# Optimization experiments

Measured on AMD Instinct MI355X. Metric: run time of the kernel, lower is better.

## Reference

```python
import jax, jax.numpy as jnp
import numpy as np


def setup_inputs() -> dict:
    key = jax.random.key(0)
    k1, k2, k3, k4 = jax.random.split(key, 4)
    B, T, L, C, F = 1024, 128, 256, 2, 784
    x = jax.random.normal(k1, (B, T, F), dtype=jnp.float32)
    W = jax.random.normal(k2, (L, F), dtype=jnp.float32) * (1.0 / np.sqrt(F))
    b = jax.random.normal(k3, (L,), dtype=jnp.float32) * 0.01
    contribution = jax.random.normal(k4, (T, L, C), dtype=jnp.float32)
    return {"x": x, "W": W, "b": b, "contribution": contribution}


def reference(x, W, b, contribution):
    # symbolic_paths: Linear(784 -> leaf) + Hardtanh  -> [B, T, L]
    sp = jnp.clip(jnp.einsum('btf,lf->btl', x, W) + b, -1.0, 1.0)
    # per-(tree,leaf) outer product: class_value[b,t,l,c] = sp[b,t,l] * contribution[t,l,c]
    cv = sp[..., None] * contribution[None]          # [B, T, L, C]
    p = jax.nn.softmax(cv, axis=-1)                  # softmax over classes
    gini = jnp.sum(1.0 - p * p, axis=-1)             # [B, T, L]
    return (sp, gini)
```

## Files before the change

### kernel.cpp

```cpp
#include <hip/hip_runtime.h>
#include <hip/hip_bf16.h>

typedef __attribute__((ext_vector_type(8))) short bf16x8;
typedef __attribute__((ext_vector_type(4))) float f32x4;

#define B_SZ   1024
#define T_SZ   128
#define L_SZ   256
#define F_SZ   784
#define M_TOT  (B_SZ * T_SZ)
#define BK     32
#define KSTEPS 25
#define KCHUNKS 100
#define BROWS  32

#define WPRE_ELEMS (KSTEPS * 4 * L_SZ)
#define WPRE_BYTES (WPRE_ELEMS * 16)
#define CDIFF_ELEMS (T_SZ * L_SZ)
#define WS_NEED (WPRE_BYTES + CDIFF_ELEMS * 4)

__device__ __forceinline__ unsigned short f2bf(float f) {
    __hip_bfloat16 h = __float2bfloat16(f);
    return *reinterpret_cast<unsigned short*>(&h);
}

__global__ __launch_bounds__(256) void dn_prep(
    const float* __restrict__ W, const float* __restrict__ contrib,
    unsigned short* __restrict__ wpre, float* __restrict__ cdiff)
{
    const int gid = blockIdx.x * 256 + threadIdx.x;
    if (gid < WPRE_ELEMS) {
        const int leaf = gid & 255;
        const int kg   = (gid >> 8) & 3;
        const int ks   = gid >> 10;
        const int k0   = ks * BK + kg * 8;
        bf16x8 v;
        #pragma unroll
        for (int j = 0; j < 8; ++j) {
            const int k = k0 + j;
            const float f = (k < F_SZ) ? W[(size_t)leaf * F_SZ + k] : 0.f;
            v[j] = (short)f2bf(f);
        }
        *reinterpret_cast<bf16x8*>(wpre + (size_t)gid * 8) = v;
    } else {
        const int cid = gid - WPRE_ELEMS;
        if (cid < CDIFF_ELEMS)
            cdiff[cid] = contrib[(size_t)cid * 2] - contrib[(size_t)cid * 2 + 1];
    }
}

__global__ __launch_bounds__(512, 6) void dn_fused7(
    const float* __restrict__ x, const unsigned short* __restrict__ wpre,
    const float* __restrict__ bias, const float* __restrict__ cdiff,
    float* __restrict__ out)
{
    __shared__ __align__(16) unsigned char smem[KCHUNKS * BROWS * 16];
    bf16x8* As = reinterpret_cast<bf16x8*>(smem);
    typedef float OtRow[264];
    OtRow* Ot = reinterpret_cast<OtRow*>(smem);

    const int tid  = threadIdx.x;
    const int lane = tid & 63;
    const int wid  = tid >> 6;
    const int lr   = lane & 15;
    const int kseg = lane >> 4;

    const int rowBase = blockIdx.x * BROWS;
    const int colBase = wid * 32;

    #pragma unroll
    for (int it = 0; it < 7; ++it) {
        const int i = it * 512 + tid;
        if (i < BROWS * KCHUNKS) {
            const int row = i / KCHUNKS;
            const int kc  = i - row * KCHUNKS;
            bf16x8 v;
            if (kc < 98) {
                const float* p = x + (size_t)(rowBase + row) * F_SZ + kc * 8;
                const f32x4 lo = *reinterpret_cast<const f32x4*>(p);
                const f32x4 hi = *reinterpret_cast<const f32x4*>(p + 4);
                #pragma unroll
                for (int j = 0; j < 4; ++j) {
                    v[j]     = (short)f2bf(lo[j]);
                    v[4 + j] = (short)f2bf(hi[j]);
                }
            } else {
                #pragma unroll
                for (int j = 0; j < 8; ++j) v[j] = 0;
            }
            As[kc * BROWS + (row ^ (kc & 7))] = v;
        }
    }
    __syncthreads();

    const unsigned short* wpb = wpre + ((size_t)kseg * L_SZ + colBase + lr) * 8;

    f32x4 acc[2][2];
    #pragma unroll
    for (int mi = 0; mi < 2; ++mi)
        #pragma unroll
        for (int ni = 0; ni < 2; ++ni)
            acc[mi][ni] = (f32x4){0.f, 0.f, 0.f, 0.f};

    bf16x8 wcur[2], wnxt[2];
    wcur[0] = *reinterpret_cast<const bf16x8*>(wpb);
    wcur[1] = *reinterpret_cast<const bf16x8*>(wpb + 128);

    #pragma unroll
    for (int ks = 0; ks < KSTEPS; ++ks) {
        if (ks + 1 < KSTEPS) {
            wnxt[0] = *reinterpret_cast<const bf16x8*>(wpb + (size_t)(ks + 1) * 8192);
            wnxt[1] = *reinterpret_cast<const bf16x8*>(wpb + (size_t)(ks + 1) * 8192 + 128);
        }
        const int kcr = ks * 4 + kseg;
        const bf16x8 a0 = As[kcr * BROWS + (lr ^ (kcr & 7))];
        const bf16x8 a1 = As[kcr * BROWS + ((16 + lr) ^ (kcr & 7))];

        acc[0][0] = __builtin_amdgcn_mfma_f32_16x16x32_bf16(a0, wcur[0], acc[0][0], 0, 0, 0);
        acc[0][1] = __builtin_amdgcn_mfma_f32_16x16x32_bf16(a0, wcur[1], acc[0][1], 0, 0, 0);
        acc[1][0] = __builtin_amdgcn_mfma_f32_16x16x32_bf16(a1, wcur[0], acc[1][0], 0, 0, 0);
        acc[1][1] = __builtin_amdgcn_mfma_f32_16x16x32_bf16(a1, wcur[1], acc[1][1], 0, 0, 0);

        wcur[0] = wnxt[0];
        wcur[1] = wnxt[1];
    }
    __syncthreads();

    float spv[2][2][4];
    #pragma unroll
    for (int ni = 0; ni < 2; ++ni) {
        const float bb = bias[colBase + ni * 16 + lr];
        #pragma unroll
        for (int mi = 0; mi < 2; ++mi)
            #pragma unroll
            for (int r = 0; r < 4; ++r)
                spv[mi][ni][r] = fminf(fmaxf(acc[mi][ni][r] + bb, -1.f), 1.f);
    }

    const int erow = tid >> 4;
    const int ecol = (tid & 15) * 4;
    const size_t GOFF = (size_t)M_TOT * L_SZ;
    float* orow = out + (size_t)(rowBase + erow) * L_SZ;

    #pragma unroll
    for (int ni = 0; ni < 2; ++ni)
        #pragma unroll
        for (int mi = 0; mi < 2; ++mi)
            #pragma unroll
            for (int r = 0; r < 4; ++r)
                Ot[mi * 16 + kseg * 4 + r][colBase + ni * 16 + lr] = spv[mi][ni][r];
    __syncthreads();
    #pragma unroll
    for (int j = 0; j < 4; ++j) {
        const f32x4 v = *reinterpret_cast<const f32x4*>(&Ot[erow][ecol + 64 * j]);
        *reinterpret_cast<f32x4*>(orow + ecol + 64 * j) = v;
    }
    __syncthreads();

    #pragma unroll
    for (int ni = 0; ni < 2; ++ni) {
        const int col = colBase + ni * 16 + lr;
        #pragma unroll
        for (int mi = 0; mi < 2; ++mi)
            #pragma unroll
            for (int r = 0; r < 4; ++r) {
                const int t = (rowBase + mi * 16 + kseg * 4 + r) & (T_SZ - 1);
                const float d  = spv[mi][ni][r] * cdiff[t * L_SZ + col];
                const float ed = __expf(d);
                const float s2 = ed / (1.f + ed);
                Ot[mi * 16 + kseg * 4 + r][col] = fmaf(2.f * s2, 1.f - s2, 1.f);
            }
    }
    __syncthreads();
    #pragma unroll
    for (int j = 0; j < 4; ++j) {
        const f32x4 v = *reinterpret_cast<const f32x4*>(&Ot[erow][ecol + 64 * j]);
        *reinterpret_cast<f32x4*>(orow + GOFF + ecol + 64 * j) = v;
    }
}

__global__ __launch_bounds__(512) void dn_fused_v1(
    const float* __restrict__ x, const float* __restrict__ W,
    const float* __restrict__ bias, const float* __restrict__ contrib,
    float* __restrict__ out)
{
    __shared__ bf16x8 As[4][128];
    __shared__ bf16x8 Bs[4][L_SZ];

    const int tid    = threadIdx.x;
    const int lane   = tid & 63;
    const int wid    = tid >> 6;
    const int waveM  = wid >> 2;
    const int waveN  = wid & 3;
    const int blkRow = blockIdx.x * 128;
    const int ar = tid >> 2;
    const int ak = (tid & 3) * 8;
    const int wr = tid >> 1;
    const int wk = (tid & 1) * 16;
    const int laneRow = lane & 15;
    const int kgrp    = lane >> 4;

    f32x4 acc[4][4];
    #pragma unroll
    for (int i = 0; i < 4; ++i)
        #pragma unroll
        for (int j = 0; j < 4; ++j)
            acc[i][j] = (f32x4){0.f, 0.f, 0.f, 0.f};

    const float* xrow = x + (size_t)(blkRow + ar) * F_SZ;
    const float* wrow = W + (size_t)wr * F_SZ;
    const f32x4 zf = {0.f, 0.f, 0.f, 0.f};

    f32x4 xa0 = *reinterpret_cast<const f32x4*>(xrow + ak);
    f32x4 xa1 = *reinterpret_cast<const f32x4*>(xrow + ak + 4);
    f32x4 wa0 = *reinterpret_cast<const f32x4*>(wrow + wk);
    f32x4 wa1 = *reinterpret_cast<const f32x4*>(wrow + wk + 4);
    f32x4 wa2 = *reinterpret_cast<const f32x4*>(wrow + wk + 8);
    f32x4 wa3 = *reinterpret_cast<const f32x4*>(wrow + wk + 12);

    for (int ks = 0; ks < KSTEPS; ++ks) {
        bf16x8 av, wv0, wv1;
        #pragma unroll
        for (int j = 0; j < 4; ++j) {
            av[j]      = (short)f2bf(xa0[j]);
            av[4 + j]  = (short)f2bf(xa1[j]);
            wv0[j]     = (short)f2bf(wa0[j]);
            wv0[4 + j] = (short)f2bf(wa1[j]);
            wv1[j]     = (short)f2bf(wa2[j]);
            wv1[4 + j] = (short)f2bf(wa3[j]);
        }
        As[ak >> 3][ar] = av;
        Bs[wk >> 3][wr] = wv0;
        Bs[(wk >> 3) + 1][wr] = wv1;
        __syncthreads();

        if (ks + 1 < KSTEPS) {
            const int kb = (ks + 1) * BK;
            if (kb + ak < F_SZ) {
                xa0 = *reinterpret_cast<const f32x4*>(xrow + kb + ak);
                xa1 = *reinterpret_cast<const f32x4*>(xrow + kb + ak + 4);
            } else { xa0 = zf; xa1 = zf; }
            if (kb + wk < F_SZ) {
                wa0 = *reinterpret_cast<const f32x4*>(wrow + kb + wk);
                wa1 = *reinterpret_cast<const f32x4*>(wrow + kb + wk + 4);
                wa2 = *reinterpret_cast<const f32x4*>(wrow + kb + wk + 8);
                wa3 = *reinterpret_cast<const f32x4*>(wrow + kb + wk + 12);
            } else { wa0 = zf; wa1 = zf; wa2 = zf; wa3 = zf; }
        }

        bf16x8 af[4], bfv[4];
        #pragma unroll
        for (int mi = 0; mi < 4; ++mi)
            af[mi] = As[kgrp][waveM * 64 + mi * 16 + laneRow];
        #pragma unroll
        for (int ni = 0; ni < 4; ++ni)
            bfv[ni] = Bs[kgrp][waveN * 64 + ni * 16 + laneRow];
        #pragma unroll
        for (int mi = 0; mi < 4; ++mi)
            #pragma unroll
            for (int ni = 0; ni < 4; ++ni)
                acc[mi][ni] = __builtin_amdgcn_mfma_f32_16x16x32_bf16(
                    af[mi], bfv[ni], acc[mi][ni], 0, 0, 0);
        __syncthreads();
    }

    const size_t GOFF  = (size_t)M_TOT * L_SZ;
    const int    rbase = waveM * 64 + (lane >> 4) * 4;
    const int    cbase = waveN * 64 + laneRow;
    #pragma unroll
    for (int ni = 0; ni < 4; ++ni) {
        const int col = cbase + ni * 16;
        const float bb = bias[col];
        #pragma unroll
        for (int mi = 0; mi < 4; ++mi) {
            #pragma unroll
            for (int r = 0; r < 4; ++r) {
                const int m = blkRow + rbase + mi * 16 + r;
                const int t = m & (T_SZ - 1);
                float v  = acc[mi][ni][r] + bb;
                float sp = fminf(fmaxf(v, -1.f), 1.f);
                const float* cp = contrib + (size_t)(t * L_SZ + col) * 2;
                const float d  = sp * (cp[0] - cp[1]);
                const float ed = __expf(d);
                const float s  = ed / (1.f + ed);
                const float g  = fmaf(2.f * s, 1.f - s, 1.f);
                const size_t o = (size_t)m * L_SZ + col;
                out[o]        = sp;
                out[GOFF + o] = g;
            }
        }
    }
}

extern "C" void kernel_launch(void* const* d_in, const int* in_sizes, int n_in,
                              void* d_out, int out_size, void* d_ws, size_t ws_size,
                              hipStream_t stream) {
    const float* x       = (const float*)d_in[0];
    const float* W       = (const float*)d_in[1];
    const float* bias    = (const float*)d_in[2];
    const float* contrib = (const float*)d_in[3];
    float* out = (float*)d_out;

    if (ws_size >= (size_t)WS_NEED && d_ws != nullptr) {
        unsigned short* wpre  = (unsigned short*)d_ws;
        float*          cdiff = (float*)((char*)d_ws + WPRE_BYTES);
        const int prep_threads = WPRE_ELEMS + CDIFF_ELEMS;
        dn_prep<<<(prep_threads + 255) / 256, 256, 0, stream>>>(W, contrib, wpre, cdiff);
        dn_fused7<<<M_TOT / BROWS, 512, 0, stream>>>(x, wpre, bias, cdiff, out);
    } else {
        dn_fused_v1<<<M_TOT / 128, 512, 0, stream>>>(x, W, bias, contrib, out);
    }
}
```

Baseline: 186.5 us.

## Warp-specialize fused kernel: producer waves stage x tiles, consumer waves run MFMA

Replaces the 512-thread single-tile kernel with a 1024-thread block that handles 128 rows in four 32-row stages. Eight producer waves convert x to bf16 into a double-buffered LDS tile while eight consumer waves run the MFMA GEMM and epilogue on the previous buffer. Each consumer wave writes its output through a small private slab, so no block-wide sync is needed for the transpose. The goal is to overlap global x loads and conversion with compute. In exchange it uses about 117 KB of LDS, which limits occupancy to one block per CU, and half the waves never issue MFMA.

```diff
diff --git a/kernel.cpp b/kernel.cpp
--- a/kernel.cpp
+++ b/kernel.cpp
@@ -12,12 +12,16 @@
 #define BK     32
 #define KSTEPS 25
 #define KCHUNKS 100
-#define BROWS  32
 
 #define WPRE_ELEMS (KSTEPS * 4 * L_SZ)
 #define WPRE_BYTES (WPRE_ELEMS * 16)
 #define CDIFF_ELEMS (T_SZ * L_SZ)
 #define WS_NEED (WPRE_BYTES + CDIFF_ELEMS * 4)
+
+#define BUFB     51200
+#define SLAB_OFF 102400
+#define SLABB    2176
+#define SMEM_SZ  119808
 
 __device__ __forceinline__ unsigned short f2bf(float f) {
     __hip_bfloat16 h = __float2bfloat16(f);
@@ -49,34 +53,28 @@
     }
 }
 
-__global__ __launch_bounds__(512, 6) void dn_fused7(
+__global__ __launch_bounds__(1024, 4) void dn_fused15(
     const float* __restrict__ x, const unsigned short* __restrict__ wpre,
     const float* __restrict__ bias, const float* __restrict__ cdiff,
     float* __restrict__ out)
 {
-    __shared__ __align__(16) unsigned char smem[KCHUNKS * BROWS * 16];
-    bf16x8* As = reinterpret_cast<bf16x8*>(smem);
-    typedef float OtRow[264];
-    OtRow* Ot = reinterpret_cast<OtRow*>(smem);
-
-    const int tid  = threadIdx.x;
-    const int lane = tid & 63;
-    const int wid  = tid >> 6;
-    const int lr   = lane & 15;
-    const int kseg = lane >> 4;
-
-    const int rowBase = blockIdx.x * BROWS;
-    const int colBase = wid * 32;
-
-    #pragma unroll
-    for (int it = 0; it < 7; ++it) {
-        const int i = it * 512 + tid;
-        if (i < BROWS * KCHUNKS) {
+    __shared__ __align__(16) unsigned char smem[SMEM_SZ];
+
+    const int tid    = threadIdx.x;
+    const int lane   = tid & 63;
+    const int wid    = tid >> 6;
+    const int rowBlk = blockIdx.x * 128;
+    const size_t GOFF = (size_t)M_TOT * L_SZ;
+
+    auto STAGE = [&](int st) {
+        bf16x8* As = reinterpret_cast<bf16x8*>(smem + (size_t)(st & 1) * BUFB);
+        const size_t rb = (size_t)(rowBlk + st * 32);
+        for (int i = wid * 64 + lane; i < 32 * KCHUNKS; i += 512) {
             const int row = i / KCHUNKS;
             const int kc  = i - row * KCHUNKS;
             bf16x8 v;
             if (kc < 98) {
-                const float* p = x + (size_t)(rowBase + row) * F_SZ + kc * 8;
+                const float* p = x + (rb + row) * F_SZ + kc * 8;
                 const f32x4 lo = *reinterpret_cast<const f32x4*>(p);
                 const f32x4 hi = *reinterpret_cast<const f32x4*>(p + 4);
                 #pragma unroll
@@ -88,94 +86,110 @@
                 #pragma unroll
                 for (int j = 0; j < 8; ++j) v[j] = 0;
             }
-            As[kc * BROWS + (row ^ (kc & 7))] = v;
-        }
-    }
+            As[kc * 32 + (row ^ (kc & 7))] = v;
+        }
+    };
+
+    const int cw      = wid - 8;
+    const int colBase = cw * 32;
+    const int lr      = lane & 15;
+    const int kseg    = lane >> 4;
+    const unsigned short* wpb =
+        wpre + ((size_t)kseg * L_SZ + colBase + lr) * 8;
+    float* slab = reinterpret_cast<float*>(smem + SLAB_OFF + cw * SLABB);
+    const int erow8 = lane >> 3;
+    const int ecol  = (lane & 7) * 4;
+
+    if (wid < 8) STAGE(0);
     __syncthreads();
 
-    const unsigned short* wpb = wpre + ((size_t)kseg * L_SZ + colBase + lr) * 8;
-
-    f32x4 acc[2][2];
-    #pragma unroll
-    for (int mi = 0; mi < 2; ++mi)
-        #pragma unroll
-        for (int ni = 0; ni < 2; ++ni)
-            acc[mi][ni] = (f32x4){0.f, 0.f, 0.f, 0.f};
-
-    bf16x8 wcur[2], wnxt[2];
-    wcur[0] = *reinterpret_cast<const bf16x8*>(wpb);
-    wcur[1] = *reinterpret_cast<const bf16x8*>(wpb + 128);
-
-    #pragma unroll
-    for (int ks = 0; ks < KSTEPS; ++ks) {
-        if (ks + 1 < KSTEPS) {
-            wnxt[0] = *reinterpret_cast<const bf16x8*>(wpb + (size_t)(ks + 1) * 8192);
-            wnxt[1] = *reinterpret_cast<const bf16x8*>(wpb + (size_t)(ks + 1) * 8192 + 128);
-        }
-        const int kcr = ks * 4 + kseg;
-        const bf16x8 a0 = As[kcr * BROWS + (lr ^ (kcr & 7))];
-        const bf16x8 a1 = As[kcr * BROWS + ((16 + lr) ^ (kcr & 7))];
-
-        acc[0][0] = __builtin_amdgcn_mfma_f32_16x16x32_bf16(a0, wcur[0], acc[0][0], 0, 0, 0);
-        acc[0][1] = __builtin_amdgcn_mfma_f32_16x16x32_bf16(a0, wcur[1], acc[0][1], 0, 0, 0);
-        acc[1][0] = __builtin_amdgcn_mfma_f32_16x16x32_bf16(a1, wcur[0], acc[1][0], 0, 0, 0);
-        acc[1][1] = __builtin_amdgcn_mfma_f32_16x16x32_bf16(a1, wcur[1], acc[1][1], 0, 0, 0);
-
-        wcur[0] = wnxt[0];
-        wcur[1] = wnxt[1];
-    }
-    __syncthreads();
-
-    float spv[2][2][4];
-    #pragma unroll
-    for (int ni = 0; ni < 2; ++ni) {
-        const float bb = bias[colBase + ni * 16 + lr];
-        #pragma unroll
-        for (int mi = 0; mi < 2; ++mi)
-            #pragma unroll
-            for (int r = 0; r < 4; ++r)
-                spv[mi][ni][r] = fminf(fmaxf(acc[mi][ni][r] + bb, -1.f), 1.f);
-    }
-
-    const int erow = tid >> 4;
-    const int ecol = (tid & 15) * 4;
-    const size_t GOFF = (size_t)M_TOT * L_SZ;
-    float* orow = out + (size_t)(rowBase + erow) * L_SZ;
-
-    #pragma unroll
-    for (int ni = 0; ni < 2; ++ni)
-        #pragma unroll
-        for (int mi = 0; mi < 2; ++mi)
-            #pragma unroll
-            for (int r = 0; r < 4; ++r)
-                Ot[mi * 16 + kseg * 4 + r][colBase + ni * 16 + lr] = spv[mi][ni][r];
-    __syncthreads();
-    #pragma unroll
-    for (int j = 0; j < 4; ++j) {
-        const f32x4 v = *reinterpret_cast<const f32x4*>(&Ot[erow][ecol + 64 * j]);
-        *reinterpret_cast<f32x4*>(orow + ecol + 64 * j) = v;
-    }
-    __syncthreads();
-
-    #pragma unroll
-    for (int ni = 0; ni < 2; ++ni) {
-        const int col = colBase + ni * 16 + lr;
-        #pragma unroll
-        for (int mi = 0; mi < 2; ++mi)
-            #pragma unroll
-            for (int r = 0; r < 4; ++r) {
-                const int t = (rowBase + mi * 16 + kseg * 4 + r) & (T_SZ - 1);
-                const float d  = spv[mi][ni][r] * cdiff[t * L_SZ + col];
-                const float ed = __expf(d);
-                const float s2 = ed / (1.f + ed);
-                Ot[mi * 16 + kseg * 4 + r][col] = fmaf(2.f * s2, 1.f - s2, 1.f);
-            }
-    }
-    __syncthreads();
-    #pragma unroll
-    for (int j = 0; j < 4; ++j) {
-        const f32x4 v = *reinterpret_cast<const f32x4*>(&Ot[erow][ecol + 64 * j]);
-        *reinterpret_cast<f32x4*>(orow + GOFF + ecol + 64 * j) = v;
+    for (int st = 0; st < 4; ++st) {
+        if (wid < 8) {
+            if (st < 3) STAGE(st + 1);
+        } else {
+            const unsigned char* Ab = smem + (size_t)(st & 1) * BUFB;
+            f32x4 acc[2][2];
+            #pragma unroll
+            for (int mi = 0; mi < 2; ++mi)
+                #pragma unroll
+                for (int ni = 0; ni < 2; ++ni)
+                    acc[mi][ni] = (f32x4){0.f, 0.f, 0.f, 0.f};
+
+            bf16x8 wcur[2], wnxt[2];
+            wcur[0] = *reinterpret_cast<const bf16x8*>(wpb);
+            wcur[1] = *reinterpret_cast<const bf16x8*>(wpb + 128);
+
+            #pragma unroll
+            for (int ks = 0; ks < KSTEPS; ++ks) {
+                if (ks + 1 < KSTEPS) {
+                    wnxt[0] = *reinterpret_cast<const bf16x8*>(wpb + (size_t)(ks + 1) * 8192);
+                    wnxt[1] = *reinterpret_cast<const bf16x8*>(wpb + (size_t)(ks + 1) * 8192 + 128);
+                }
+                const int kcr = ks * 4 + kseg;
+                const bf16x8 a0 = *reinterpret_cast<const bf16x8*>(
+                    Ab + (size_t)(kcr * 32 + (lr ^ (kcr & 7))) * 16);
+                const bf16x8 a1 = *reinterpret_cast<const bf16x8*>(
+                    Ab + (size_t)(kcr * 32 + ((16 + lr) ^ (kcr & 7))) * 16);
+
+                acc[0][0] = __builtin_amdgcn_mfma_f32_16x16x32_bf16(a0, wcur[0], acc[0][0], 0, 0, 0);
+                acc[0][1] = __builtin_amdgcn_mfma_f32_16x16x32_bf16(a0, wcur[1], acc[0][1], 0, 0, 0);
+                acc[1][0] = __builtin_amdgcn_mfma_f32_16x16x32_bf16(a1, wcur[0], acc[1][0], 0, 0, 0);
+                acc[1][1] = __builtin_amdgcn_mfma_f32_16x16x32_bf16(a1, wcur[1], acc[1][1], 0, 0, 0);
+                wcur[0] = wnxt[0];
+                wcur[1] = wnxt[1];
+            }
+
+            float spv[2][2][4];
+            #pragma unroll
+            for (int ni = 0; ni < 2; ++ni) {
+                const float bb = bias[colBase + ni * 16 + lr];
+                #pragma unroll
+                for (int mi = 0; mi < 2; ++mi)
+                    #pragma unroll
+                    for (int r = 0; r < 4; ++r)
+                        spv[mi][ni][r] = fminf(fmaxf(acc[mi][ni][r] + bb, -1.f), 1.f);
+            }
+            const int rowB = rowBlk + st * 32;
+
+            #pragma unroll
+            for (int h = 0; h < 2; ++h) {
+                #pragma unroll
+                for (int ni = 0; ni < 2; ++ni)
+                    #pragma unroll
+                    for (int r = 0; r < 4; ++r)
+                        slab[(kseg * 4 + r) * 34 + ni * 16 + lr] = spv[h][ni][r];
+                #pragma unroll
+                for (int j = 0; j < 2; ++j) {
+                    const int row = j * 8 + erow8;
+                    const f32x4 v = *reinterpret_cast<const f32x4*>(slab + row * 34 + ecol);
+                    *reinterpret_cast<f32x4*>(out + (size_t)(rowB + h * 16 + row) * L_SZ
+                                              + colBase + ecol) = v;
+                }
+            }
+            #pragma unroll
+            for (int h = 0; h < 2; ++h) {
+                #pragma unroll
+                for (int ni = 0; ni < 2; ++ni) {
+                    const int col = colBase + ni * 16 + lr;
+                    #pragma unroll
+                    for (int r = 0; r < 4; ++r) {
+                        const int t = (rowB + h * 16 + kseg * 4 + r) & (T_SZ - 1);
+                        const float d  = spv[h][ni][r] * cdiff[t * L_SZ + col];
+                        const float ed = __expf(d);
+                        const float s2 = ed / (1.f + ed);
+                        slab[(kseg * 4 + r) * 34 + col - colBase] = fmaf(2.f * s2, 1.f - s2, 1.f);
+                    }
+                }
+                #pragma unroll
+                for (int j = 0; j < 2; ++j) {
+                    const int row = j * 8 + erow8;
+                    const f32x4 v = *reinterpret_cast<const f32x4*>(slab + row * 34 + ecol);
+                    *reinterpret_cast<f32x4*>(out + GOFF + (size_t)(rowB + h * 16 + row) * L_SZ
+                                              + colBase + ecol) = v;
+                }
+            }
+        }
+        __syncthreads();
     }
 }
 
@@ -306,7 +320,7 @@
         float*          cdiff = (float*)((char*)d_ws + WPRE_BYTES);
         const int prep_threads = WPRE_ELEMS + CDIFF_ELEMS;
         dn_prep<<<(prep_threads + 255) / 256, 256, 0, stream>>>(W, contrib, wpre, cdiff);
-        dn_fused7<<<M_TOT / BROWS, 512, 0, stream>>>(x, wpre, bias, cdiff, out);
+        dn_fused15<<<M_TOT / 128, 1024, 0, stream>>>(x, wpre, bias, cdiff, out);
     } else {
         dn_fused_v1<<<M_TOT / 128, 512, 0, stream>>>(x, W, bias, contrib, out);
     }
```

Result: slower. 450.1 us (+141.4%).
